# Kernel tuning notes

Hardware: AMD Instinct MI355X
Metric: run time of the kernel (lower is better)

Reference implementation:

```python
import jax, jax.numpy as jnp
import numpy as np

# dims
B = 2
HC, WC = 96, 96      # coarse spatial
HF, WF = 384, 384
CIN_C = 256          # in_coarser_channels
CIN_F = 3            # in_finer_channels
CH = 64              # hidden_channels
COUT = 19            # out_channels
KS, DIL = 3, 1       # local attention window


def conv2d(x, w, b=None, pad=0):
    y = jax.lax.conv_general_dilated(
        x, w, window_strides=(1, 1), padding=[(pad, pad), (pad, pad)],
        dimension_numbers=("NCHW", "OIHW", "NCHW"))
    if b is not None:
        y = y + b[None, :, None, None]
    return y


def upsample_nearest(x, factor):
    return jnp.repeat(jnp.repeat(x, factor, axis=2), factor, axis=3)


def local_attn_2d(q, k, v, kernel_size=KS, dilation=DIL):
    # per-pixel attention over a (kernel_size x kernel_size) dilated neighborhood
    Bq, C, H, W = q.shape
    Cv = v.shape[1]
    pad = dilation * (kernel_size - 1) // 2
    kp = jnp.pad(k, ((0, 0), (0, 0), (pad, pad), (pad, pad)))
    vp = jnp.pad(v, ((0, 0), (0, 0), (pad, pad), (pad, pad)))
    offs = [(i * dilation, j * dilation)
            for i in range(kernel_size) for j in range(kernel_size)]
    # scores: (B, K*K, H, W) -- q . k_neighbor per offset (zero-padded borders)
    scores = jnp.stack(
        [(q * kp[:, :, oi:oi + H, oj:oj + W]).sum(axis=1) for oi, oj in offs],
        axis=1)
    attn = jax.nn.softmax(scores, axis=1)
    y = jnp.zeros((Bq, Cv, H, W), q.dtype)
    for idx, (oi, oj) in enumerate(offs):
        y = y + attn[:, idx:idx + 1] * vp[:, :, oi:oi + H, oj:oj + W]
    return y


def setup_inputs() -> dict:
    key = jax.random.key(0)
    ks = jax.random.split(key, 11)
    p = lambda i, shape: jax.random.normal(ks[i], shape, jnp.float32) * 0.05
    return dict(
        coarse_feature=jax.random.normal(ks[0], (B, CIN_C, HC, WC), jnp.float32),
        raw_image=jax.random.uniform(ks[1], (B, CIN_F, HF, WF), jnp.float32),
        w_ef=p(2, (1, CIN_F, 3, 3)), b_ef=p(3, (1,)),          # edge_finer conv3x3
        w_ec=p(4, (CH, CIN_C, 3, 3)), b_ec=p(5, (CH,)),        # edge_coarser conv3x3
        w_eh=p(6, (1, CH + 1, 1, 1)),                          # edge_head conv1x1, no bias
        w_q=p(7, (CH, CIN_F, 1, 1)), b_q=p(8, (CH,)),          # xq_head conv1x1
        w_v=p(9, (COUT, CIN_C + CH, 1, 1)), b_v=p(10, (COUT,)) # xv_head conv1x1
    )


def reference(coarse_feature, raw_image, w_ef, b_ef, w_ec, b_ec, w_eh,
              w_q, b_q, w_v, b_v):
    f = HF // HC
    # edge branch
    ef = jax.nn.relu(conv2d(raw_image, w_ef, b_ef, pad=1))           # (B,1,HF,WF)
    ec = jax.nn.relu(conv2d(coarse_feature, w_ec, b_ec, pad=1))      # (B,CH,HC,WC)
    edge_logit = conv2d(jnp.concatenate([upsample_nearest(ec, f), ef], axis=1), w_eh)
    non_edge = jax.nn.sigmoid(edge_logit)                            # (B,1,HF,WF)
    # q / k / v
    xq = conv2d(raw_image, w_q, b_q)                                 # (B,CH,HF,WF)
    xk = non_edge * xq
    xv = conv2d(jnp.concatenate([upsample_nearest(coarse_feature, f), xq], axis=1),
                w_v, b_v)                                            # (B,COUT,HF,WF)
    y = local_attn_2d(xq, xk, xv)
    return y, non_edge
```

## Files before the change

kernel.cpp:

```cpp
#include <hip/hip_runtime.h>
#include <math.h>

#define B_    2
#define HC_   96
#define WC_   96
#define HF_   384
#define WF_   384
#define CINC_ 256
#define CH_   64
#define COUT_ 19

typedef __attribute__((ext_vector_type(8))) short bf16x8;
typedef __attribute__((ext_vector_type(4))) float f32x4;

__device__ __forceinline__ unsigned short f2bf(float f) {
    unsigned int u = __float_as_uint(f);
    u += 0x7fffu + ((u >> 16) & 1u);
    return (unsigned short)(u >> 16);
}
__device__ __forceinline__ unsigned int pk2(float a, float b) {
    return (unsigned int)f2bf(a) | ((unsigned int)f2bf(b) << 16);
}
__device__ __forceinline__ float bflo(unsigned int u) { return __uint_as_float(u << 16); }
__device__ __forceinline__ float bfhi(unsigned int u) { return __uint_as_float(u & 0xffff0000u); }

__device__ __forceinline__ void gl_lds16(const void* g, void* l) {
    __builtin_amdgcn_global_load_lds(
        (const __attribute__((address_space(1))) void*)g,
        (__attribute__((address_space(3))) void*)l, 16, 0, 0);
}

__global__ __launch_bounds__(256) void k_pre(
    const float* __restrict__ x,
    const float* __restrict__ w_ec, const float* __restrict__ w_v,
    const float* __restrict__ w_q,  const float* __restrict__ b_q,
    const float* __restrict__ b_v,
    unsigned short* __restrict__ Xt,
    unsigned short* __restrict__ A_pk, unsigned short* __restrict__ Avc,
    float* __restrict__ drv)
{
    const int bid = blockIdx.x;
    const int tid = threadIdx.x;
    if (bid < 576) {
        int i = bid * 256 + tid;
        {
            int e = i & 7, l = (i >> 3) & 63, m = (i >> 9) & 3, ck = (i >> 11) & 7, tap = i >> 14;
            int oc = m * 16 + (l & 15);
            int ch = ck * 32 + (l >> 4) * 8 + e;
            A_pk[i] = f2bf(w_ec[(oc * 256 + ch) * 9 + tap]);
        }
        if (i < 8192) {
            int e = i & 7, l = (i >> 3) & 63, m = (i >> 9) & 1, ck = (i >> 10) & 7;
            int ov = m * 16 + (l & 15);
            int ch = ck * 32 + (l >> 4) * 8 + e;
            Avc[i] = (ov < COUT_) ? f2bf(w_v[ov * 320 + ch]) : (unsigned short)0;
        }
        return;
    }
    if (bid < 580) {
        int e = (bid - 576) * 256 + tid;
        if (e >= 388 * B_) return;
        int b = e / 388, i = e - b * 388;
        int gy, gx;
        if (i < 98)       { gy = 0;           gx = i; }
        else if (i < 196) { gy = 97;          gx = i - 98; }
        else if (i < 292) { gy = i - 196 + 1; gx = 0; }
        else              { gy = i - 292 + 1; gx = 97; }
        uint4* dst = (uint4*)(Xt + (((size_t)(b * 98 + gy)) * 98 + gx) * 256);
        uint4 zz; zz.x = zz.y = zz.z = zz.w = 0u;
        #pragma unroll
        for (int c = 0; c < 32; ++c) dst[c] = zz;
        return;
    }
    if (bid < 1156) {
        int u = bid - 580;
        int bx = u % 36;
        int rb = u / 36;
        int b  = rb & 1;
        int cz = (rb >> 1) * 32;
        int px = bx * 256 + tid;
        int gy = px / 96, gx = px - gy * 96;
        const float* src = x + (size_t)b * CINC_ * 9216;
        unsigned short* dst = Xt + (((size_t)(b * 98 + gy + 1)) * 98 + gx + 1) * 256;
        for (int c0 = cz; c0 < cz + 32; c0 += 8) {
            float f[8];
            #pragma unroll
            for (int t = 0; t < 8; ++t) f[t] = src[(size_t)(c0 + t) * 9216 + px];
            uint4 v;
            v.x = pk2(f[0], f[1]);
            v.y = pk2(f[2], f[3]);
            v.z = pk2(f[4], f[5]);
            v.w = pk2(f[6], f[7]);
            *(uint4*)&dst[c0] = v;
        }
        return;
    }
    {
        int i = tid;
        if (i < 9) {
            int ci = i / 3, cj = i % 3;
            float a = 0.f;
            for (int c = 0; c < 64; ++c) a += w_q[c * 3 + ci] * w_q[c * 3 + cj];
            drv[i] = a;
        } else if (i < 12) {
            int ci = i - 9;
            float a = 0.f;
            for (int c = 0; c < 64; ++c) a += w_q[c * 3 + ci] * b_q[c];
            drv[i] = a;
        } else if (i == 12) {
            float a = 0.f;
            for (int c = 0; c < 64; ++c) a += b_q[c] * b_q[c];
            drv[12] = a;
        } else if (i < 70) {
            int idx = i - 13, ci = idx / 19, ov = idx % 19;
            float a = 0.f;
            for (int c = 0; c < 64; ++c) a += w_v[ov * 320 + 256 + c] * w_q[c * 3 + ci];
            drv[i] = a;
        } else if (i < 89) {
            int ov = i - 70;
            float a = b_v[ov];
            for (int c = 0; c < 64; ++c) a += w_v[ov * 320 + 256 + c] * b_q[c];
            drv[i] = a;
        }
        return;
    }
}

__global__ __launch_bounds__(256, 2) void k_ec(
    const unsigned short* __restrict__ Xt,
    const unsigned short* __restrict__ A_pk,
    const unsigned short* __restrict__ Avc,
    const float* __restrict__ b_ec, const float* __restrict__ w_eh,
    float* __restrict__ eh4,
    float* __restrict__ cvb)
{
    __shared__ uint4 sB[4][768];

    const int tid  = threadIdx.x;
    const int lane = tid & 63;
    const int wv   = tid >> 6;
    const int j    = lane & 15;
    const int g    = lane >> 4;
    const int zb   = blockIdx.z;
    const int z    = zb & 3;
    const int b    = zb >> 2;
    const int ty0  = blockIdx.y * 8;
    const int tx0  = blockIdx.x * 16;

    f32x4 acc0 = (f32x4)0.f, acc1 = (f32x4)0.f;
    f32x4 accv[2][2];
    accv[0][0] = accv[0][1] = accv[1][0] = accv[1][1] = (f32x4)0.f;

    const bf16x8* Af  = (const bf16x8*)A_pk;
    const bf16x8* Avf = (const bf16x8*)Avc;

#define STAGE_EC(BUF, CK)                                                      \
    {                                                                          \
        _Pragma("unroll")                                                      \
        for (int rr = 0; rr < 3; ++rr) {                                       \
            int slot = 192 * wv + 64 * rr + lane;                              \
            int px = slot >> 2;                                                \
            px = px > 179 ? 179 : px;                                          \
            int part = (slot & 3) ^ ((px >> 1) & 3);                           \
            int row = px / 18, col = px - row * 18;                            \
            const unsigned short* src = Xt                                     \
                + (((size_t)(b * 98 + ty0 + row)) * 98 + (tx0 + col)) * 256    \
                + (CK) * 32 + part * 8;                                        \
            gl_lds16(src, &sB[BUF][192 * wv + 64 * rr]);                       \
        }                                                                      \
    }

    STAGE_EC(0, 0);
    STAGE_EC(1, 1);

    #pragma unroll
    for (int ck = 0; ck < 8; ++ck) {
        if (ck < 6) STAGE_EC((ck + 2) & 3, ck + 2);

        if (ck < 6)       asm volatile("s_waitcnt vmcnt(6)" ::: "memory");
        else if (ck == 6) asm volatile("s_waitcnt vmcnt(3)" ::: "memory");
        else              asm volatile("s_waitcnt vmcnt(0)" ::: "memory");
        __builtin_amdgcn_sched_barrier(0);
        asm volatile("s_barrier" ::: "memory");

        const int cur = ck & 3;
        bf16x8 frg[4][3];
        #pragma unroll
        for (int rr = 0; rr < 4; ++rr)
            #pragma unroll
            for (int dx = 0; dx < 3; ++dx) {
                int px = (2 * wv + rr) * 18 + j + dx;
                int slot = (px << 2) + (g ^ ((px >> 1) & 3));
                frg[rr][dx] = *(const bf16x8*)&sB[cur][slot];
            }

        #pragma unroll
        for (int tap = 0; tap < 9; ++tap) {
            const int dy = tap / 3, dx = tap % 3;
            bf16x8 a = Af[((tap * 8 + ck) * 4 + z) * 64 + lane];
            acc0 = __builtin_amdgcn_mfma_f32_16x16x32_bf16(a, frg[dy][dx], acc0, 0, 0, 0);
            acc1 = __builtin_amdgcn_mfma_f32_16x16x32_bf16(a, frg[dy + 1][dx], acc1, 0, 0, 0);
        }
        if (z == 0) {
            bf16x8 av0 = Avf[(ck * 2 + 0) * 64 + lane];
            bf16x8 av1 = Avf[(ck * 2 + 1) * 64 + lane];
            accv[0][0] = __builtin_amdgcn_mfma_f32_16x16x32_bf16(av0, frg[1][1], accv[0][0], 0, 0, 0);
            accv[0][1] = __builtin_amdgcn_mfma_f32_16x16x32_bf16(av0, frg[2][1], accv[0][1], 0, 0, 0);
            accv[1][0] = __builtin_amdgcn_mfma_f32_16x16x32_bf16(av1, frg[1][1], accv[1][0], 0, 0, 0);
            accv[1][1] = __builtin_amdgcn_mfma_f32_16x16x32_bf16(av1, frg[2][1], accv[1][1], 0, 0, 0);
        }
    }
#undef STAGE_EC

    float we[4], be[4];
    #pragma unroll
    for (int q = 0; q < 4; ++q) {
        int oc = z * 16 + 4 * g + q;
        we[q] = w_eh[oc];
        be[q] = b_ec[oc];
    }
    #pragma unroll
    for (int r = 0; r < 2; ++r) {
        const f32x4 accr = r ? acc1 : acc0;
        float p = 0.f;
        #pragma unroll
        for (int q = 0; q < 4; ++q)
            p += we[q] * fmaxf(accr[q] + be[q], 0.f);
        p += __shfl_xor(p, 16);
        p += __shfl_xor(p, 32);
        const int gpix = (ty0 + 2 * wv + r) * WC_ + tx0 + j;
        if (g == 0)
            eh4[((size_t)b * (HC_ * WC_) + gpix) * 4 + z] = p;
        if (z == 0) {
            float* cvp = cvb + ((size_t)b * (HC_ * WC_) + gpix) * 20;
            #pragma unroll
            for (int m = 0; m < 2; ++m)
                #pragma unroll
                for (int q = 0; q < 4; ++q) {
                    int ov = m * 16 + 4 * g + q;
                    if (ov < 20) cvp[ov] = accv[m][r][q];
                }
        }
    }
}

__global__ __launch_bounds__(512, 6) void k_fine(
    const float* __restrict__ raw,
    const float* __restrict__ w_ef, const float* __restrict__ b_ef,
    const float* __restrict__ w_eh,
    const float* __restrict__ drv,
    const float* __restrict__ eh4,
    const float* __restrict__ cvb,
    float* __restrict__ out_y,
    float* __restrict__ out_ne)
{
    __shared__ float sRaw[3][20][36];
    __shared__ unsigned short sV[612 * 26];
    __shared__ float sNE[612];

    const int tid = threadIdx.x;
    const int b   = blockIdx.z;
    const int ty0 = blockIdx.y * 16;
    const int tx0 = blockIdx.x * 32;
    const float* rb = raw + (size_t)b * 3 * (HF_ * WF_);

    const float* Gm = drv;
    const float* uv = drv + 9;
    const float* Mm = drv + 13;
    const float* bc = drv + 70;

    for (int i = tid; i < 2160; i += 512) {
        int ch = i / 720, rem = i - ch * 720;
        int ry = rem / 36, rx = rem - ry * 36;
        int gh = ty0 + ry - 2, gw = tx0 + rx - 2;
        float v = 0.f;
        if (gh >= 0 && gh < HF_ && gw >= 0 && gw < WF_)
            v = rb[(size_t)ch * (HF_ * WF_) + gh * WF_ + gw];
        sRaw[ch][ry][rx] = v;
    }
    __syncthreads();

    for (int p = tid; p < 612; p += 512) {
        const int iy = p / 34, ix = p - iy * 34;
        const int gh = ty0 + iy - 1, gw = tx0 + ix - 1;
        unsigned int* vw = (unsigned int*)&sV[p * 26];
        if (gh < 0 || gh >= HF_ || gw < 0 || gw >= WF_) {
            #pragma unroll
            for (int w = 0; w < 10; ++w) vw[w] = 0u;
            sNE[p] = 0.f;
            continue;
        }
        float ef = b_ef[0];
        #pragma unroll
        for (int ci = 0; ci < 3; ++ci)
            #pragma unroll
            for (int t = 0; t < 9; ++t)
                ef = fmaf(w_ef[ci * 9 + t], sRaw[ci][iy + t / 3][ix + t % 3], ef);
        ef = fmaxf(ef, 0.f);

        const int cpix = (gh >> 2) * WC_ + (gw >> 2);
        const float4 ehv = *(const float4*)(eh4 + ((size_t)b * (HC_ * WC_) + cpix) * 4);
        float logit = fmaf(w_eh[64], ef, (ehv.x + ehv.y) + (ehv.z + ehv.w));
        float ne = 1.f / (1.f + __expf(-logit));
        sNE[p] = ne;

        const float r0 = sRaw[0][iy + 1][ix + 1];
        const float r1 = sRaw[1][iy + 1][ix + 1];
        const float r2 = sRaw[2][iy + 1][ix + 1];

        float v[20];
        {
            const float4* cvp = (const float4*)(cvb + ((size_t)b * (HC_ * WC_) + cpix) * 20);
            float4 c0 = cvp[0], c1 = cvp[1], c2 = cvp[2], c3 = cvp[3], c4 = cvp[4];
            v[0] = c0.x; v[1] = c0.y; v[2] = c0.z; v[3] = c0.w;
            v[4] = c1.x; v[5] = c1.y; v[6] = c1.z; v[7] = c1.w;
            v[8] = c2.x; v[9] = c2.y; v[10] = c2.z; v[11] = c2.w;
            v[12] = c3.x; v[13] = c3.y; v[14] = c3.z; v[15] = c3.w;
            v[16] = c4.x; v[17] = c4.y; v[18] = c4.z;
        }
        #pragma unroll
        for (int ov = 0; ov < COUT_; ++ov)
            v[ov] = fmaf(Mm[38 + ov], r2,
                    fmaf(Mm[19 + ov], r1,
                    fmaf(Mm[ov], r0, v[ov] + bc[ov])));

        #pragma unroll
        for (int o2 = 0; o2 < 9; ++o2)
            vw[o2] = pk2(v[2 * o2], v[2 * o2 + 1]);
        vw[9] = (unsigned int)f2bf(v[18]);
    }
    __syncthreads();

    const int py = tid >> 5, px2 = tid & 31;
    const int iy = py + 1, ix = px2 + 1;
    const int pbase = iy * 34 + ix;

    float rn[3][9];
    #pragma unroll
    for (int ci = 0; ci < 3; ++ci)
        #pragma unroll
        for (int k = 0; k < 9; ++k)
            rn[ci][k] = sRaw[ci][iy + k / 3][ix + k % 3];

    const float rc0 = rn[0][4], rc1 = rn[1][4], rc2 = rn[2][4];
    const float h0 = fmaf(Gm[0], rc0, fmaf(Gm[1], rc1, fmaf(Gm[2], rc2, uv[0])));
    const float h1 = fmaf(Gm[3], rc0, fmaf(Gm[4], rc1, fmaf(Gm[5], rc2, uv[1])));
    const float h2 = fmaf(Gm[6], rc0, fmaf(Gm[7], rc1, fmaf(Gm[8], rc2, uv[2])));
    const float ac = fmaf(uv[0], rc0, fmaf(uv[1], rc1, fmaf(uv[2], rc2, drv[12])));

    float sc[9];
    #pragma unroll
    for (int k = 0; k < 9; ++k) {
        float d = fmaf(h0, rn[0][k], fmaf(h1, rn[1][k], fmaf(h2, rn[2][k], ac)));
        const int pn = pbase + (k / 3 - 1) * 34 + (k % 3 - 1);
        sc[k] = sNE[pn] * d;
    }
    float mmax = sc[0];
    #pragma unroll
    for (int k = 1; k < 9; ++k) mmax = fmaxf(mmax, sc[k]);
    float e[9];
    float ssum = 0.f;
    #pragma unroll
    for (int k = 0; k < 9; ++k) { e[k] = __expf(sc[k] - mmax); ssum += e[k]; }
    const float inv = 1.f / ssum;

    float y[COUT_];
    #pragma unroll
    for (int ov = 0; ov < COUT_; ++ov) y[ov] = 0.f;
    #pragma unroll
    for (int k = 0; k < 9; ++k) {
        const int pn = pbase + (k / 3 - 1) * 34 + (k % 3 - 1);
        const float a = e[k] * inv;
        const unsigned int* vp = (const unsigned int*)&sV[pn * 26];
        #pragma unroll
        for (int o2 = 0; o2 < 9; ++o2) {
            unsigned int u = vp[o2];
            y[2 * o2]     = fmaf(a, bflo(u), y[2 * o2]);
            y[2 * o2 + 1] = fmaf(a, bfhi(u), y[2 * o2 + 1]);
        }
        y[18] = fmaf(a, bflo(vp[9]), y[18]);
    }

    const int gh = ty0 + py, gw = tx0 + px2;
    const size_t ppos = (size_t)gh * WF_ + gw;
    #pragma unroll
    for (int ov = 0; ov < COUT_; ++ov)
        out_y[((size_t)b * COUT_ + ov) * (HF_ * WF_) + ppos] = y[ov];
    out_ne[(size_t)b * (HF_ * WF_) + ppos] = sNE[pbase];
}

extern "C" void kernel_launch(void* const* d_in, const int* in_sizes, int n_in,
                              void* d_out, int out_size, void* d_ws, size_t ws_size,
                              hipStream_t stream)
{
    const float* coarse = (const float*)d_in[0];
    const float* raw    = (const float*)d_in[1];
    const float* w_ef   = (const float*)d_in[2];
    const float* b_ef   = (const float*)d_in[3];
    const float* w_ec   = (const float*)d_in[4];
    const float* b_ec   = (const float*)d_in[5];
    const float* w_eh   = (const float*)d_in[6];
    const float* w_q    = (const float*)d_in[7];
    const float* b_q    = (const float*)d_in[8];
    const float* w_v    = (const float*)d_in[9];
    const float* b_v    = (const float*)d_in[10];
    (void)in_sizes; (void)n_in; (void)out_size; (void)ws_size;

    unsigned char* ws = (unsigned char*)d_ws;
    size_t off = 0;
    unsigned short* Xt    = (unsigned short*)(ws + off); off += (size_t)B_ * 98 * 98 * 256 * 2;
    unsigned short* A_pk  = (unsigned short*)(ws + off); off += 294912;
    unsigned short* Avc   = (unsigned short*)(ws + off); off += 16384;
    float* eh4    = (float*)(ws + off); off += (size_t)B_ * 9216 * 4 * 4;
    float* cvb    = (float*)(ws + off); off += (size_t)B_ * 9216 * 20 * 4;
    float* drv    = (float*)(ws + off); off += 512;

    float* out_y  = (float*)d_out;
    float* out_ne = out_y + (size_t)B_ * COUT_ * HF_ * WF_;

    hipLaunchKernelGGL(k_pre, dim3(1157), dim3(256), 0, stream,
                       coarse, w_ec, w_v, w_q, b_q, b_v, Xt, A_pk, Avc, drv);
    hipLaunchKernelGGL(k_ec, dim3(6, 12, 4 * B_), dim3(256), 0, stream,
                       Xt, A_pk, Avc, b_ec, w_eh, eh4, cvb);
    hipLaunchKernelGGL(k_fine, dim3(12, 24, B_), dim3(512), 0, stream,
                       raw, w_ef, b_ef, w_eh, drv, eh4, cvb, out_y, out_ne);
}
```

Measured before the change: 52.89 us.

## Use chunk-major Xt layout, XCD-aware tile mapping, and bf16 cvb buffer

Changes the padded bf16 coarse-feature buffer from pixel-major with 256 channels contiguous to chunk-major (8-channel chunks, each a plane of pixels). This makes both the k_pre transpose stores and the k_ec LDS staging loads contiguous across neighbouring pixels. Replaces the 3D k_ec grid with a flat grid remapped so that the four channel-group blocks of each tile land on the same XCD, which is meant to improve L2 reuse. Also stores the intermediate value buffer cvb as bf16 with 24-element stride instead of fp32, halving that traffic at the cost of extra rounding in the v path.

```diff
diff --git a/kernel.cpp b/kernel.cpp
--- a/kernel.cpp
+++ b/kernel.cpp
@@ -30,12 +30,14 @@
         (__attribute__((address_space(3))) void*)l, 16, 0, 0);
 }
 
+#define XT_IDX(b, chunk, hpx)  (((size_t)((b) * 32 + (chunk))) * 9604 + (hpx))
+
 __global__ __launch_bounds__(256) void k_pre(
     const float* __restrict__ x,
     const float* __restrict__ w_ec, const float* __restrict__ w_v,
     const float* __restrict__ w_q,  const float* __restrict__ b_q,
     const float* __restrict__ b_v,
-    unsigned short* __restrict__ Xt,
+    uint4* __restrict__ Xt4,
     unsigned short* __restrict__ A_pk, unsigned short* __restrict__ Avc,
     float* __restrict__ drv)
 {
@@ -66,32 +68,34 @@
         else if (i < 196) { gy = 97;          gx = i - 98; }
         else if (i < 292) { gy = i - 196 + 1; gx = 0; }
         else              { gy = i - 292 + 1; gx = 97; }
-        uint4* dst = (uint4*)(Xt + (((size_t)(b * 98 + gy)) * 98 + gx) * 256);
+        const int hpx = gy * 98 + gx;
         uint4 zz; zz.x = zz.y = zz.z = zz.w = 0u;
         #pragma unroll
-        for (int c = 0; c < 32; ++c) dst[c] = zz;
+        for (int c = 0; c < 32; ++c) Xt4[XT_IDX(b, c, hpx)] = zz;
         return;
     }
     if (bid < 1156) {
         int u = bid - 580;
         int bx = u % 36;
-        int rb = u / 36;
-        int b  = rb & 1;
-        int cz = (rb >> 1) * 32;
+        int v2 = u / 36;
+        int cg = v2 & 7;
+        int b  = v2 >> 3;
         int px = bx * 256 + tid;
         int gy = px / 96, gx = px - gy * 96;
-        const float* src = x + (size_t)b * CINC_ * 9216;
-        unsigned short* dst = Xt + (((size_t)(b * 98 + gy + 1)) * 98 + gx + 1) * 256;
-        for (int c0 = cz; c0 < cz + 32; c0 += 8) {
+        const int hpx = (gy + 1) * 98 + gx + 1;
+        const float* src = x + (size_t)b * CINC_ * 9216 + px;
+        #pragma unroll
+        for (int cc = 0; cc < 4; ++cc) {
+            const int chunk = cg * 4 + cc;
             float f[8];
             #pragma unroll
-            for (int t = 0; t < 8; ++t) f[t] = src[(size_t)(c0 + t) * 9216 + px];
+            for (int t = 0; t < 8; ++t) f[t] = src[(size_t)(chunk * 8 + t) * 9216];
             uint4 v;
             v.x = pk2(f[0], f[1]);
             v.y = pk2(f[2], f[3]);
             v.z = pk2(f[4], f[5]);
             v.w = pk2(f[6], f[7]);
-            *(uint4*)&dst[c0] = v;
+            Xt4[XT_IDX(b, chunk, hpx)] = v;
         }
         return;
     }
@@ -127,12 +131,12 @@
 }
 
 __global__ __launch_bounds__(256, 2) void k_ec(
-    const unsigned short* __restrict__ Xt,
+    const uint4* __restrict__ Xt4,
     const unsigned short* __restrict__ A_pk,
     const unsigned short* __restrict__ Avc,
     const float* __restrict__ b_ec, const float* __restrict__ w_eh,
     float* __restrict__ eh4,
-    float* __restrict__ cvb)
+    unsigned short* __restrict__ cvb)
 {
     __shared__ uint4 sB[4][768];
 
@@ -141,11 +145,17 @@
     const int wv   = tid >> 6;
     const int j    = lane & 15;
     const int g    = lane >> 4;
-    const int zb   = blockIdx.z;
-    const int z    = zb & 3;
-    const int b    = zb >> 2;
-    const int ty0  = blockIdx.y * 8;
-    const int tx0  = blockIdx.x * 16;
+
+    const int flat = blockIdx.x;
+    const int xcd  = flat & 7;
+    const int slot0 = flat >> 3;
+    const int z    = slot0 & 3;
+    const int t8   = slot0 >> 2;
+    const int tile = t8 * 8 + xcd;
+    const int b    = tile / 72;
+    const int tl   = tile - b * 72;
+    const int ty0  = (tl / 6) * 8;
+    const int tx0  = (tl % 6) * 16;
 
     f32x4 acc0 = (f32x4)0.f, acc1 = (f32x4)0.f;
     f32x4 accv[2][2];
@@ -163,9 +173,8 @@
             px = px > 179 ? 179 : px;                                          \
             int part = (slot & 3) ^ ((px >> 1) & 3);                           \
             int row = px / 18, col = px - row * 18;                            \
-            const unsigned short* src = Xt                                     \
-                + (((size_t)(b * 98 + ty0 + row)) * 98 + (tx0 + col)) * 256    \
-                + (CK) * 32 + part * 8;                                        \
+            const uint4* src = Xt4 + XT_IDX(b, (CK) * 4 + part,                \
+                                            (ty0 + row) * 98 + (tx0 + col));   \
             gl_lds16(src, &sB[BUF][192 * wv + 64 * rr]);                       \
         }                                                                      \
     }
@@ -232,13 +241,13 @@
         if (g == 0)
             eh4[((size_t)b * (HC_ * WC_) + gpix) * 4 + z] = p;
         if (z == 0) {
-            float* cvp = cvb + ((size_t)b * (HC_ * WC_) + gpix) * 20;
+            unsigned short* cvp = cvb + ((size_t)b * (HC_ * WC_) + gpix) * 24;
             #pragma unroll
             for (int m = 0; m < 2; ++m)
                 #pragma unroll
                 for (int q = 0; q < 4; ++q) {
                     int ov = m * 16 + 4 * g + q;
-                    if (ov < 20) cvp[ov] = accv[m][r][q];
+                    if (ov < 20) cvp[ov] = f2bf(accv[m][r][q]);
                 }
         }
     }
@@ -250,7 +259,7 @@
     const float* __restrict__ w_eh,
     const float* __restrict__ drv,
     const float* __restrict__ eh4,
-    const float* __restrict__ cvb,
+    const unsigned short* __restrict__ cvb,
     float* __restrict__ out_y,
     float* __restrict__ out_ne)
 {
@@ -310,13 +319,15 @@
 
         float v[20];
         {
-            const float4* cvp = (const float4*)(cvb + ((size_t)b * (HC_ * WC_) + cpix) * 20);
-            float4 c0 = cvp[0], c1 = cvp[1], c2 = cvp[2], c3 = cvp[3], c4 = cvp[4];
-            v[0] = c0.x; v[1] = c0.y; v[2] = c0.z; v[3] = c0.w;
-            v[4] = c1.x; v[5] = c1.y; v[6] = c1.z; v[7] = c1.w;
-            v[8] = c2.x; v[9] = c2.y; v[10] = c2.z; v[11] = c2.w;
-            v[12] = c3.x; v[13] = c3.y; v[14] = c3.z; v[15] = c3.w;
-            v[16] = c4.x; v[17] = c4.y; v[18] = c4.z;
+            const uint4* cvp = (const uint4*)(cvb + ((size_t)b * (HC_ * WC_) + cpix) * 24);
+            uint4 a0 = cvp[0], a1 = cvp[1];
+            uint4 a2 = cvp[2];
+            unsigned int w10[10] = {a0.x, a0.y, a0.z, a0.w, a1.x, a1.y, a1.z, a1.w, a2.x, a2.y};
+            #pragma unroll
+            for (int o2 = 0; o2 < 10; ++o2) {
+                v[2 * o2]     = bflo(w10[o2]);
+                v[2 * o2 + 1] = bfhi(w10[o2]);
+            }
         }
         #pragma unroll
         for (int ov = 0; ov < COUT_; ++ov)
@@ -408,20 +419,20 @@
 
     unsigned char* ws = (unsigned char*)d_ws;
     size_t off = 0;
-    unsigned short* Xt    = (unsigned short*)(ws + off); off += (size_t)B_ * 98 * 98 * 256 * 2;
+    uint4* Xt4            = (uint4*)(ws + off);          off += (size_t)B_ * 32 * 9604 * 16;
     unsigned short* A_pk  = (unsigned short*)(ws + off); off += 294912;
     unsigned short* Avc   = (unsigned short*)(ws + off); off += 16384;
-    float* eh4    = (float*)(ws + off); off += (size_t)B_ * 9216 * 4 * 4;
-    float* cvb    = (float*)(ws + off); off += (size_t)B_ * 9216 * 20 * 4;
-    float* drv    = (float*)(ws + off); off += 512;
+    float* eh4            = (float*)(ws + off);          off += (size_t)B_ * 9216 * 4 * 4;
+    unsigned short* cvb   = (unsigned short*)(ws + off); off += (size_t)B_ * 9216 * 24 * 2;
+    float* drv            = (float*)(ws + off);          off += 512;
 
     float* out_y  = (float*)d_out;
     float* out_ne = out_y + (size_t)B_ * COUT_ * HF_ * WF_;
 
     hipLaunchKernelGGL(k_pre, dim3(1157), dim3(256), 0, stream,
-                       coarse, w_ec, w_v, w_q, b_q, b_v, Xt, A_pk, Avc, drv);
-    hipLaunchKernelGGL(k_ec, dim3(6, 12, 4 * B_), dim3(256), 0, stream,
-                       Xt, A_pk, Avc, b_ec, w_eh, eh4, cvb);
+                       coarse, w_ec, w_v, w_q, b_q, b_v, Xt4, A_pk, Avc, drv);
+    hipLaunchKernelGGL(k_ec, dim3(576), dim3(256), 0, stream,
+                       Xt4, A_pk, Avc, b_ec, w_eh, eh4, cvb);
     hipLaunchKernelGGL(k_fine, dim3(12, 24, B_), dim3(512), 0, stream,
                        raw, w_ef, b_ef, w_eh, drv, eh4, cvb, out_y, out_ne);
 }
```

Result: faster. 45.52 us (-13.9%).
